# Performance work log

Hardware: AMD Instinct MI355X
Metric: run time of the kernel (lower is better)

Reference implementation:

```python
import jax, jax.numpy as jnp
import numpy as np

N_NODES = 100000
D = 256            # in_channels
H = 256            # hidden_channels
E = 1000000        # number of query pairs


def setup_inputs() -> dict:
    key = jax.random.key(0)
    ks = jax.random.split(key, 8)
    x = jax.random.normal(ks[0], (N_NODES, D), dtype=jnp.float32)
    edge_index = jax.random.randint(ks[1], (2, 1000), 0, N_NODES, dtype=jnp.int64)
    edge_pairs = jax.random.randint(ks[2], (E, 2), 0, N_NODES, dtype=jnp.int64)
    # MLP params (Linear stores y = x @ W + b, W shaped [in, out])
    s1 = 1.0 / np.sqrt(D)
    s2 = 1.0 / np.sqrt(H)
    s3 = 1.0 / np.sqrt(H // 2)
    W1 = jax.random.uniform(ks[3], (D, H), jnp.float32, -s1, s1)
    b1 = jnp.zeros((H,), jnp.float32)
    W2 = jax.random.uniform(ks[4], (H, H // 2), jnp.float32, -s2, s2)
    b2 = jnp.zeros((H // 2,), jnp.float32)
    W3 = jax.random.uniform(ks[5], (H // 2, 1), jnp.float32, -s3, s3)
    b3 = jnp.zeros((1,), jnp.float32)
    return {"x": x, "W1": W1, "b1": b1, "W2": W2, "b2": b2,
            "W3": W3, "b3": b3, "edge_index": edge_index, "edge_pairs": edge_pairs}


def reference(x, W1, b1, W2, b2, W3, b3, edge_index, edge_pairs):
    # Gather node pairs and form elementwise-product pair features [E, D]
    feats = x[edge_pairs[:, 0]] * x[edge_pairs[:, 1]]
    # 3-layer MLP (dropout inactive at inference)
    h = jax.nn.relu(feats @ W1 + b1)
    h = jax.nn.relu(h @ W2 + b2)
    scores = h @ W3 + b3
    return scores.reshape(-1)
```

## Files before the change

kernel.cpp:

```cpp
#include <hip/hip_runtime.h>


typedef __attribute__((ext_vector_type(8))) short short8;
typedef __attribute__((ext_vector_type(4))) float floatx4;
typedef __attribute__((ext_vector_type(4))) unsigned uintx4;
typedef __attribute__((ext_vector_type(2))) int intx2;

#define MT 64
#define NTHREADS 512
#define NBLOCKS 256

__device__ __forceinline__ unsigned short f2bf(float f) {
  union { float f; unsigned u; } a; a.f = f;
  unsigned r = a.u + 0x7FFFu + ((a.u >> 16) & 1u);
  return (unsigned short)(r >> 16);
}

__device__ __forceinline__ unsigned pkbf(float lo, float hi) {
  unsigned r;
  asm("v_cvt_pk_bf16_f32 %0, %1, %2" : "=v"(r) : "v"(lo), "v"(hi));
  return r;
}

__device__ __forceinline__ unsigned bfmul2(unsigned ua, unsigned ub) {
  float lo = __uint_as_float(ua << 16)          * __uint_as_float(ub << 16);
  float hi = __uint_as_float(ua & 0xFFFF0000u) * __uint_as_float(ub & 0xFFFF0000u);
  return pkbf(lo, hi);
}

__global__ void prep_kernel(const float* __restrict__ x,
                            const float* __restrict__ W1,
                            const float* __restrict__ W2,
                            unsigned short* __restrict__ xb,
                            unsigned short* __restrict__ w1t,
                            unsigned short* __restrict__ w2t, int n4) {
  int i = blockIdx.x * blockDim.x + threadIdx.x;
  if (i < n4) {
    float4 v = ((const float4*)x)[i];
    ushort4 o;
    o.x = f2bf(v.x); o.y = f2bf(v.y); o.z = f2bf(v.z); o.w = f2bf(v.w);
    ((ushort4*)xb)[i] = o;
  } else {
    int j = i - n4;
    if (j < 256 * 256) {
      int k = j >> 8, n = j & 255;
      w1t[n * 256 + k] = f2bf(W1[k * 256 + n]);
    } else {
      j -= 256 * 256;
      if (j < 128 * 256) {
        int p = j >> 7, n = j & 127;
        int kp = (p & ~31) | ((p & 1) << 4) | ((p & 31) >> 1);
        w2t[n * 256 + p] = f2bf(W2[kp * 128 + n]);
      }
    }
  }
}

__global__ __launch_bounds__(NTHREADS, 2) void mlp_kernel(
    const unsigned short* __restrict__ xb,
    const unsigned short* __restrict__ w1t,
    const unsigned short* __restrict__ w2t,
    const float* __restrict__ b1,
    const float* __restrict__ b2,
    const float* __restrict__ w3,
    const float* __restrict__ b3,
    const int* __restrict__ ep,
    float* __restrict__ out,
    int E)
{
  __shared__ __align__(16) unsigned short feats[2][MT * 256];
  __shared__ __align__(16) unsigned short h1b[MT * 256];
  __shared__ __align__(16) float part[MT][4];

  const int tid  = threadIdx.x;
  const int wv   = tid >> 6;
  const int lane = tid & 63;
  const int q    = lane >> 4;
  const int r16  = lane & 15;
  const int c    = tid & 31;
  const int mrow = tid >> 5;
  const int mg   = wv >> 2;
  const int cg   = wv & 3;

  const int ntiles = (E + MT - 1) / MT;
  const int b = blockIdx.x;
  const int nloc = (ntiles - 1 - b) / NBLOCKS + 1;

  short8 w1r[2][8], w2r[2][8];
  float b1r[2], b2r[2], w3r[2];
  #pragma unroll
  for (int ct = 0; ct < 2; ++ct) {
    const int n1 = wv * 32 + ct * 16 + r16;
    const unsigned short* p1 = w1t + n1 * 256 + q * 8;
    #pragma unroll
    for (int kt = 0; kt < 8; ++kt) w1r[ct][kt] = *(const short8*)(p1 + kt * 32);
    b1r[ct] = b1[n1];
    const int n2 = cg * 32 + ct * 16 + r16;
    const unsigned short* p2 = w2t + n2 * 256 + q * 8;
    #pragma unroll
    for (int kt = 0; kt < 8; ++kt) w2r[ct][kt] = *(const short8*)(p2 + kt * 32);
    b2r[ct] = b2[n2];
    w3r[ct] = w3[n2];
  }
  const float b3v = b3[0];

  intx2 uv0, uv1, uv2, uv3;
  {
    #pragma unroll
    for (int s = 0; s < 4; ++s) {
      int m = mrow + 16 * s;
      int g = b * MT + m;
      intx2 uv = __builtin_nontemporal_load((const intx2*)(ep + 2 * (size_t)g));
      uintx4 a  = *(const uintx4*)(xb + ((size_t)(unsigned)uv.x << 8) + (c << 3));
      uintx4 bv = *(const uintx4*)(xb + ((size_t)(unsigned)uv.y << 8) + (c << 3));
      uintx4 pv;
      #pragma unroll
      for (int tt = 0; tt < 4; ++tt) pv[tt] = bfmul2(a[tt], bv[tt]);
      *(uintx4*)((char*)feats[0] + m * 512 + ((c ^ (m & 15)) << 4)) = pv;
    }
    const int t1 = b + NBLOCKS;
    uv0 = __builtin_nontemporal_load((const intx2*)(ep + 2 * (size_t)(t1 * MT + mrow)));
    uv1 = __builtin_nontemporal_load((const intx2*)(ep + 2 * (size_t)(t1 * MT + mrow + 16)));
    uv2 = __builtin_nontemporal_load((const intx2*)(ep + 2 * (size_t)(t1 * MT + mrow + 32)));
    uv3 = __builtin_nontemporal_load((const intx2*)(ep + 2 * (size_t)(t1 * MT + mrow + 48)));
  }
  __syncthreads();

  for (int i = 0; i < nloc; ++i) {
    const int fp = i & 1;
    const bool stg = (i + 1 < nloc);

    if (stg) {
      uintx4 ra0 = *(const uintx4*)(xb + ((size_t)(unsigned)uv0.x << 8) + (c << 3));
      uintx4 rb0 = *(const uintx4*)(xb + ((size_t)(unsigned)uv0.y << 8) + (c << 3));
      uintx4 ra1 = *(const uintx4*)(xb + ((size_t)(unsigned)uv1.x << 8) + (c << 3));
      uintx4 rb1 = *(const uintx4*)(xb + ((size_t)(unsigned)uv1.y << 8) + (c << 3));
      uintx4 ra2 = *(const uintx4*)(xb + ((size_t)(unsigned)uv2.x << 8) + (c << 3));
      uintx4 rb2 = *(const uintx4*)(xb + ((size_t)(unsigned)uv2.y << 8) + (c << 3));
      uintx4 ra3 = *(const uintx4*)(xb + ((size_t)(unsigned)uv3.x << 8) + (c << 3));
      uintx4 rb3 = *(const uintx4*)(xb + ((size_t)(unsigned)uv3.y << 8) + (c << 3));

      {
        const int t2 = b + (i + 2) * NBLOCKS;
        int g0 = t2 * MT + mrow;      if (g0 >= E) g0 = E - 1;
        int g1 = t2 * MT + mrow + 16; if (g1 >= E) g1 = E - 1;
        int g2 = t2 * MT + mrow + 32; if (g2 >= E) g2 = E - 1;
        int g3 = t2 * MT + mrow + 48; if (g3 >= E) g3 = E - 1;
        uv0 = __builtin_nontemporal_load((const intx2*)(ep + 2 * (size_t)g0));
        uv1 = __builtin_nontemporal_load((const intx2*)(ep + 2 * (size_t)g1));
        uv2 = __builtin_nontemporal_load((const intx2*)(ep + 2 * (size_t)g2));
        uv3 = __builtin_nontemporal_load((const intx2*)(ep + 2 * (size_t)g3));
      }

      char* const bufn = (char*)feats[fp ^ 1];
      uintx4 pv;
      int m = mrow;
      #pragma unroll
      for (int tt = 0; tt < 4; ++tt) pv[tt] = bfmul2(ra0[tt], rb0[tt]);
      *(uintx4*)(bufn + m * 512 + ((c ^ (m & 15)) << 4)) = pv;
      m = mrow + 16;
      #pragma unroll
      for (int tt = 0; tt < 4; ++tt) pv[tt] = bfmul2(ra1[tt], rb1[tt]);
      *(uintx4*)(bufn + m * 512 + ((c ^ (m & 15)) << 4)) = pv;
      m = mrow + 32;
      #pragma unroll
      for (int tt = 0; tt < 4; ++tt) pv[tt] = bfmul2(ra2[tt], rb2[tt]);
      *(uintx4*)(bufn + m * 512 + ((c ^ (m & 15)) << 4)) = pv;
      m = mrow + 48;
      #pragma unroll
      for (int tt = 0; tt < 4; ++tt) pv[tt] = bfmul2(ra3[tt], rb3[tt]);
      *(uintx4*)(bufn + m * 512 + ((c ^ (m & 15)) << 4)) = pv;
    }

    floatx4 acc[4][2];
    #pragma unroll
    for (int mt = 0; mt < 4; ++mt) {
      acc[mt][0] = (floatx4){0.f, 0.f, 0.f, 0.f};
      acc[mt][1] = (floatx4){0.f, 0.f, 0.f, 0.f};
    }
    const char* const a1base = (const char*)feats[fp] + r16 * 512;
    #pragma unroll
    for (int kt = 0; kt < 8; ++kt) {
      const int aoff = (kt << 6) ^ ((q ^ r16) << 4);
      #pragma unroll
      for (int mt = 0; mt < 4; ++mt) {
        short8 av = *(const short8*)(a1base + mt * (16 * 512) + aoff);
        acc[mt][0] = __builtin_amdgcn_mfma_f32_16x16x32_bf16(av, w1r[0][kt], acc[mt][0], 0, 0, 0);
        acc[mt][1] = __builtin_amdgcn_mfma_f32_16x16x32_bf16(av, w1r[1][kt], acc[mt][1], 0, 0, 0);
      }
    }

    {
      char* const hb = (char*)h1b;
      const int chp = wv * 4 + (r16 >> 2);
      const int ino = (r16 & 3) << 2;
      #pragma unroll
      for (int mt = 0; mt < 4; ++mt) {
        #pragma unroll
        for (int r = 0; r < 4; ++r) {
          const int m = mt * 16 + q * 4 + r;
          unsigned pk = pkbf(fmaxf(acc[mt][0][r] + b1r[0], 0.f),
                             fmaxf(acc[mt][1][r] + b1r[1], 0.f));
          *(unsigned*)(hb + m * 512 + ((chp ^ (m & 15)) << 4) + ino) = pk;
        }
      }
    }
    __syncthreads();

    floatx4 acc2[2][2];
    acc2[0][0] = (floatx4){0.f, 0.f, 0.f, 0.f};
    acc2[0][1] = (floatx4){0.f, 0.f, 0.f, 0.f};
    acc2[1][0] = (floatx4){0.f, 0.f, 0.f, 0.f};
    acc2[1][1] = (floatx4){0.f, 0.f, 0.f, 0.f};
    const char* const a2base = (const char*)h1b + (mg * 32 + r16) * 512;
    #pragma unroll
    for (int kt = 0; kt < 8; ++kt) {
      const int aoff = (kt << 6) ^ ((q ^ r16) << 4);
      short8 av0 = *(const short8*)(a2base + aoff);
      short8 av1 = *(const short8*)(a2base + 16 * 512 + aoff);
      acc2[0][0] = __builtin_amdgcn_mfma_f32_16x16x32_bf16(av0, w2r[0][kt], acc2[0][0], 0, 0, 0);
      acc2[0][1] = __builtin_amdgcn_mfma_f32_16x16x32_bf16(av0, w2r[1][kt], acc2[0][1], 0, 0, 0);
      acc2[1][0] = __builtin_amdgcn_mfma_f32_16x16x32_bf16(av1, w2r[0][kt], acc2[1][0], 0, 0, 0);
      acc2[1][1] = __builtin_amdgcn_mfma_f32_16x16x32_bf16(av1, w2r[1][kt], acc2[1][1], 0, 0, 0);
    }

    #pragma unroll
    for (int mt = 0; mt < 2; ++mt) {
      #pragma unroll
      for (int r = 0; r < 4; ++r) {
        float pp = fmaxf(acc2[mt][0][r] + b2r[0], 0.f) * w3r[0]
                 + fmaxf(acc2[mt][1][r] + b2r[1], 0.f) * w3r[1];
        pp += __shfl_xor(pp, 1);
        pp += __shfl_xor(pp, 2);
        pp += __shfl_xor(pp, 4);
        pp += __shfl_xor(pp, 8);
        if (r16 == 0)
          part[mg * 32 + mt * 16 + q * 4 + r][cg] = pp;
      }
    }
    __syncthreads();

    if (tid < MT) {
      floatx4 pr = *(const floatx4*)part[tid];
      out[(size_t)(b + i * NBLOCKS) * MT + tid] =
          (pr[0] + pr[1]) + (pr[2] + pr[3]) + b3v;
    }
  }
}

extern "C" void kernel_launch(void* const* d_in, const int* in_sizes, int n_in,
                              void* d_out, int out_size, void* d_ws, size_t ws_size,
                              hipStream_t stream) {
  const float* x  = (const float*)d_in[0];
  const float* W1 = (const float*)d_in[1];
  const float* b1 = (const float*)d_in[2];
  const float* W2 = (const float*)d_in[3];
  const float* b2 = (const float*)d_in[4];
  const float* W3 = (const float*)d_in[5];
  const float* b3 = (const float*)d_in[6];
  const int*   ep = (const int*)d_in[8];
  float* out = (float*)d_out;

  const int NX = in_sizes[0];
  const int E  = in_sizes[8] / 2;

  unsigned short* xb  = (unsigned short*)d_ws;
  unsigned short* w1t = (unsigned short*)((char*)d_ws + (size_t)NX * 2);
  unsigned short* w2t = w1t + 256 * 256;

  const int n4 = NX / 4;
  const int prep_threads = n4 + 256 * 256 + 128 * 256;
  prep_kernel<<<(prep_threads + 255) / 256, 256, 0, stream>>>(x, W1, W2, xb, w1t, w2t, n4);
  mlp_kernel<<<NBLOCKS, NTHREADS, 0, stream>>>(xb, w1t, w2t, b1, b2, W3, b3, ep, out, E);
}
```

Before: 448.0 us.

## Software-pipeline MLP layers across tiles with one barrier per iteration

Restructures the per-tile loop into a three-stage software pipeline. Layer 1 of tile i, layer 2 of tile i-1 and the output write of tile i-2 now run in the same iteration, using double-buffered h1 and partial-sum LDS buffers, so only one __syncthreads per iteration is needed instead of two. Layer 1 is split into two 32-row halves to cut accumulator registers, and the gather loads are issued before layer-1 compute so their latency is hidden. This adds extra LDS use and two drain iterations, and may raise register pressure, which could hurt occupancy at 2 blocks per CU.

```diff
diff --git a/kernel.cpp b/kernel.cpp
--- a/kernel.cpp
+++ b/kernel.cpp
@@ -69,8 +69,8 @@
     int E)
 {
   __shared__ __align__(16) unsigned short feats[2][MT * 256];
-  __shared__ __align__(16) unsigned short h1b[MT * 256];
-  __shared__ __align__(16) float part[MT][4];
+  __shared__ __align__(16) unsigned short h1b[2][MT * 256];
+  __shared__ __align__(16) float part[2][MT][4];
 
   const int tid  = threadIdx.x;
   const int wv   = tid >> 6;
@@ -126,32 +126,60 @@
   }
   __syncthreads();
 
-  for (int i = 0; i < nloc; ++i) {
+  for (int i = 0; i <= nloc + 1; ++i) {
     const int fp = i & 1;
     const bool stg = (i + 1 < nloc);
 
+    uintx4 ra0, rb0, ra1, rb1, ra2, rb2, ra3, rb3;
     if (stg) {
-      uintx4 ra0 = *(const uintx4*)(xb + ((size_t)(unsigned)uv0.x << 8) + (c << 3));
-      uintx4 rb0 = *(const uintx4*)(xb + ((size_t)(unsigned)uv0.y << 8) + (c << 3));
-      uintx4 ra1 = *(const uintx4*)(xb + ((size_t)(unsigned)uv1.x << 8) + (c << 3));
-      uintx4 rb1 = *(const uintx4*)(xb + ((size_t)(unsigned)uv1.y << 8) + (c << 3));
-      uintx4 ra2 = *(const uintx4*)(xb + ((size_t)(unsigned)uv2.x << 8) + (c << 3));
-      uintx4 rb2 = *(const uintx4*)(xb + ((size_t)(unsigned)uv2.y << 8) + (c << 3));
-      uintx4 ra3 = *(const uintx4*)(xb + ((size_t)(unsigned)uv3.x << 8) + (c << 3));
-      uintx4 rb3 = *(const uintx4*)(xb + ((size_t)(unsigned)uv3.y << 8) + (c << 3));
-
-      {
-        const int t2 = b + (i + 2) * NBLOCKS;
-        int g0 = t2 * MT + mrow;      if (g0 >= E) g0 = E - 1;
-        int g1 = t2 * MT + mrow + 16; if (g1 >= E) g1 = E - 1;
-        int g2 = t2 * MT + mrow + 32; if (g2 >= E) g2 = E - 1;
-        int g3 = t2 * MT + mrow + 48; if (g3 >= E) g3 = E - 1;
-        uv0 = __builtin_nontemporal_load((const intx2*)(ep + 2 * (size_t)g0));
-        uv1 = __builtin_nontemporal_load((const intx2*)(ep + 2 * (size_t)g1));
-        uv2 = __builtin_nontemporal_load((const intx2*)(ep + 2 * (size_t)g2));
-        uv3 = __builtin_nontemporal_load((const intx2*)(ep + 2 * (size_t)g3));
-      }
-
+      ra0 = *(const uintx4*)(xb + ((size_t)(unsigned)uv0.x << 8) + (c << 3));
+      rb0 = *(const uintx4*)(xb + ((size_t)(unsigned)uv0.y << 8) + (c << 3));
+      ra1 = *(const uintx4*)(xb + ((size_t)(unsigned)uv1.x << 8) + (c << 3));
+      rb1 = *(const uintx4*)(xb + ((size_t)(unsigned)uv1.y << 8) + (c << 3));
+      ra2 = *(const uintx4*)(xb + ((size_t)(unsigned)uv2.x << 8) + (c << 3));
+      rb2 = *(const uintx4*)(xb + ((size_t)(unsigned)uv2.y << 8) + (c << 3));
+      ra3 = *(const uintx4*)(xb + ((size_t)(unsigned)uv3.x << 8) + (c << 3));
+      rb3 = *(const uintx4*)(xb + ((size_t)(unsigned)uv3.y << 8) + (c << 3));
+    }
+
+    if (i < nloc) {
+      char* const hb = (char*)h1b[fp];
+      const int chp = wv * 4 + (r16 >> 2);
+      const int ino = (r16 & 3) << 2;
+      #pragma unroll
+      for (int mh = 0; mh < 2; ++mh) {
+        floatx4 acc[2][2];
+        #pragma unroll
+        for (int mt = 0; mt < 2; ++mt) {
+          acc[mt][0] = (floatx4){0.f, 0.f, 0.f, 0.f};
+          acc[mt][1] = (floatx4){0.f, 0.f, 0.f, 0.f};
+        }
+        const char* const a1base =
+            (const char*)feats[fp] + r16 * 512 + mh * (32 * 512);
+        #pragma unroll
+        for (int kt = 0; kt < 8; ++kt) {
+          const int aoff = (kt << 6) ^ ((q ^ r16) << 4);
+          #pragma unroll
+          for (int mt = 0; mt < 2; ++mt) {
+            short8 av = *(const short8*)(a1base + mt * (16 * 512) + aoff);
+            acc[mt][0] = __builtin_amdgcn_mfma_f32_16x16x32_bf16(av, w1r[0][kt], acc[mt][0], 0, 0, 0);
+            acc[mt][1] = __builtin_amdgcn_mfma_f32_16x16x32_bf16(av, w1r[1][kt], acc[mt][1], 0, 0, 0);
+          }
+        }
+        #pragma unroll
+        for (int mt = 0; mt < 2; ++mt) {
+          #pragma unroll
+          for (int r = 0; r < 4; ++r) {
+            const int m = mh * 32 + mt * 16 + q * 4 + r;
+            unsigned pk = pkbf(fmaxf(acc[mt][0][r] + b1r[0], 0.f),
+                               fmaxf(acc[mt][1][r] + b1r[1], 0.f));
+            *(unsigned*)(hb + m * 512 + ((chp ^ (m & 15)) << 4) + ino) = pk;
+          }
+        }
+      }
+    }
+
+    if (stg) {
       char* const bufn = (char*)feats[fp ^ 1];
       uintx4 pv;
       int m = mrow;
@@ -170,81 +198,59 @@
       #pragma unroll
       for (int tt = 0; tt < 4; ++tt) pv[tt] = bfmul2(ra3[tt], rb3[tt]);
       *(uintx4*)(bufn + m * 512 + ((c ^ (m & 15)) << 4)) = pv;
-    }
-
-    floatx4 acc[4][2];
-    #pragma unroll
-    for (int mt = 0; mt < 4; ++mt) {
-      acc[mt][0] = (floatx4){0.f, 0.f, 0.f, 0.f};
-      acc[mt][1] = (floatx4){0.f, 0.f, 0.f, 0.f};
-    }
-    const char* const a1base = (const char*)feats[fp] + r16 * 512;
-    #pragma unroll
-    for (int kt = 0; kt < 8; ++kt) {
-      const int aoff = (kt << 6) ^ ((q ^ r16) << 4);
-      #pragma unroll
-      for (int mt = 0; mt < 4; ++mt) {
-        short8 av = *(const short8*)(a1base + mt * (16 * 512) + aoff);
-        acc[mt][0] = __builtin_amdgcn_mfma_f32_16x16x32_bf16(av, w1r[0][kt], acc[mt][0], 0, 0, 0);
-        acc[mt][1] = __builtin_amdgcn_mfma_f32_16x16x32_bf16(av, w1r[1][kt], acc[mt][1], 0, 0, 0);
-      }
-    }
-
-    {
-      char* const hb = (char*)h1b;
-      const int chp = wv * 4 + (r16 >> 2);
-      const int ino = (r16 & 3) << 2;
-      #pragma unroll
-      for (int mt = 0; mt < 4; ++mt) {
+
+      const int t2 = b + (i + 2) * NBLOCKS;
+      int g0 = t2 * MT + mrow;      if (g0 >= E) g0 = E - 1;
+      int g1 = t2 * MT + mrow + 16; if (g1 >= E) g1 = E - 1;
+      int g2 = t2 * MT + mrow + 32; if (g2 >= E) g2 = E - 1;
+      int g3 = t2 * MT + mrow + 48; if (g3 >= E) g3 = E - 1;
+      uv0 = __builtin_nontemporal_load((const intx2*)(ep + 2 * (size_t)g0));
+      uv1 = __builtin_nontemporal_load((const intx2*)(ep + 2 * (size_t)g1));
+      uv2 = __builtin_nontemporal_load((const intx2*)(ep + 2 * (size_t)g2));
+      uv3 = __builtin_nontemporal_load((const intx2*)(ep + 2 * (size_t)g3));
+    }
+
+    if (i >= 1 && i <= nloc) {
+      floatx4 acc2[2][2];
+      acc2[0][0] = (floatx4){0.f, 0.f, 0.f, 0.f};
+      acc2[0][1] = (floatx4){0.f, 0.f, 0.f, 0.f};
+      acc2[1][0] = (floatx4){0.f, 0.f, 0.f, 0.f};
+      acc2[1][1] = (floatx4){0.f, 0.f, 0.f, 0.f};
+      const char* const a2base =
+          (const char*)h1b[fp ^ 1] + (mg * 32 + r16) * 512;
+      #pragma unroll
+      for (int kt = 0; kt < 8; ++kt) {
+        const int aoff = (kt << 6) ^ ((q ^ r16) << 4);
+        short8 av0 = *(const short8*)(a2base + aoff);
+        short8 av1 = *(const short8*)(a2base + 16 * 512 + aoff);
+        acc2[0][0] = __builtin_amdgcn_mfma_f32_16x16x32_bf16(av0, w2r[0][kt], acc2[0][0], 0, 0, 0);
+        acc2[0][1] = __builtin_amdgcn_mfma_f32_16x16x32_bf16(av0, w2r[1][kt], acc2[0][1], 0, 0, 0);
+        acc2[1][0] = __builtin_amdgcn_mfma_f32_16x16x32_bf16(av1, w2r[0][kt], acc2[1][0], 0, 0, 0);
+        acc2[1][1] = __builtin_amdgcn_mfma_f32_16x16x32_bf16(av1, w2r[1][kt], acc2[1][1], 0, 0, 0);
+      }
+      #pragma unroll
+      for (int mt = 0; mt < 2; ++mt) {
         #pragma unroll
         for (int r = 0; r < 4; ++r) {
-          const int m = mt * 16 + q * 4 + r;
-          unsigned pk = pkbf(fmaxf(acc[mt][0][r] + b1r[0], 0.f),
-                             fmaxf(acc[mt][1][r] + b1r[1], 0.f));
-          *(unsigned*)(hb + m * 512 + ((chp ^ (m & 15)) << 4) + ino) = pk;
-        }
-      }
-    }
+          float pp = fmaxf(acc2[mt][0][r] + b2r[0], 0.f) * w3r[0]
+                   + fmaxf(acc2[mt][1][r] + b2r[1], 0.f) * w3r[1];
+          pp += __shfl_xor(pp, 1);
+          pp += __shfl_xor(pp, 2);
+          pp += __shfl_xor(pp, 4);
+          pp += __shfl_xor(pp, 8);
+          if (r16 == 0)
+            part[fp ^ 1][mg * 32 + mt * 16 + q * 4 + r][cg] = pp;
+        }
+      }
+    }
+
+    if (i >= 2 && tid < MT) {
+      floatx4 pr = *(const floatx4*)part[fp][tid];
+      out[(size_t)(b + (i - 2) * NBLOCKS) * MT + tid] =
+          (pr[0] + pr[1]) + (pr[2] + pr[3]) + b3v;
+    }
+
     __syncthreads();
-
-    floatx4 acc2[2][2];
-    acc2[0][0] = (floatx4){0.f, 0.f, 0.f, 0.f};
-    acc2[0][1] = (floatx4){0.f, 0.f, 0.f, 0.f};
-    acc2[1][0] = (floatx4){0.f, 0.f, 0.f, 0.f};
-    acc2[1][1] = (floatx4){0.f, 0.f, 0.f, 0.f};
-    const char* const a2base = (const char*)h1b + (mg * 32 + r16) * 512;
-    #pragma unroll
-    for (int kt = 0; kt < 8; ++kt) {
-      const int aoff = (kt << 6) ^ ((q ^ r16) << 4);
-      short8 av0 = *(const short8*)(a2base + aoff);
-      short8 av1 = *(const short8*)(a2base + 16 * 512 + aoff);
-      acc2[0][0] = __builtin_amdgcn_mfma_f32_16x16x32_bf16(av0, w2r[0][kt], acc2[0][0], 0, 0, 0);
-      acc2[0][1] = __builtin_amdgcn_mfma_f32_16x16x32_bf16(av0, w2r[1][kt], acc2[0][1], 0, 0, 0);
-      acc2[1][0] = __builtin_amdgcn_mfma_f32_16x16x32_bf16(av1, w2r[0][kt], acc2[1][0], 0, 0, 0);
-      acc2[1][1] = __builtin_amdgcn_mfma_f32_16x16x32_bf16(av1, w2r[1][kt], acc2[1][1], 0, 0, 0);
-    }
-
-    #pragma unroll
-    for (int mt = 0; mt < 2; ++mt) {
-      #pragma unroll
-      for (int r = 0; r < 4; ++r) {
-        float pp = fmaxf(acc2[mt][0][r] + b2r[0], 0.f) * w3r[0]
-                 + fmaxf(acc2[mt][1][r] + b2r[1], 0.f) * w3r[1];
-        pp += __shfl_xor(pp, 1);
-        pp += __shfl_xor(pp, 2);
-        pp += __shfl_xor(pp, 4);
-        pp += __shfl_xor(pp, 8);
-        if (r16 == 0)
-          part[mg * 32 + mt * 16 + q * 4 + r][cg] = pp;
-      }
-    }
-    __syncthreads();
-
-    if (tid < MT) {
-      floatx4 pr = *(const floatx4*)part[tid];
-      out[(size_t)(b + i * NBLOCKS) * MT + tid] =
-          (pr[0] + pr[1]) + (pr[2] + pr[3]) + b3v;
-    }
   }
 }
 
```

After: 439.0 us. 2.0% less time.
